# Performance work log

Hardware: AMD Instinct MI355X
Metric: run time of the kernel (lower is better)

## Reference

```python
import jax, jax.numpy as jnp
import numpy as np

NUM_HEADS = 8


def _attn(q, k, v, scale):
    # q: [B,H,Nq,d], k/v: [B,H,Nk,d]
    a = jax.nn.softmax(jnp.einsum('bhqd,bhkd->bhqk', q, k) * scale, axis=-1)
    return jnp.einsum('bhqk,bhkd->bhqd', a, v)


def setup_inputs() -> dict:
    key = jax.random.key(0)
    k1, k2, k3 = jax.random.split(key, 3)
    B, N, C = 8, 1024, 768
    x = jax.random.normal(k1, (B, N, C), dtype=jnp.float32)
    w_qkv = jax.random.normal(k2, (3 * C, C), dtype=jnp.float32) * 0.02
    w_proj = jax.random.normal(k3, (C, C), dtype=jnp.float32) * 0.02
    b_proj = jnp.zeros((C,), dtype=jnp.float32)
    return {"x": x, "w_qkv": w_qkv, "w_proj": w_proj, "b_proj": b_proj}


def reference(x, w_qkv, w_proj, b_proj):
    B, N, C = x.shape
    H = NUM_HEADS
    hd = C // H            # full head dim (scale uses this, per the source)
    g = hd // 3            # per-group head dim
    scale = hd ** (-0.5)

    qkv = (x @ w_qkv.T).reshape(B, N, 3, H, hd).transpose(2, 0, 3, 1, 4)  # [3,B,H,N,hd]
    q, k, v = qkv[0], qkv[1], qkv[2]

    q3, q4, q5 = q[..., :g], q[..., g:2 * g], q[..., 2 * g:]
    k3, k4, k5 = k[..., :g], k[..., g:2 * g], k[..., 2 * g:]
    v3, v4, v5 = v[..., :g], v[..., g:2 * g], v[..., 2 * g:]

    def merge(o):  # [B,H,N,g] -> [B,N,H*g]
        return o.transpose(0, 2, 1, 3).reshape(B, N, C // 3)

    x3 = merge(_attn(q4, jnp.concatenate([k3, k4], axis=2), jnp.concatenate([v3, v4], axis=2), scale))
    x4 = merge(_attn(q5, jnp.concatenate([k3, k5], axis=2), jnp.concatenate([v3, v5], axis=2), scale))
    x5 = merge(_attn(q5, jnp.concatenate([k4, k5], axis=2), jnp.concatenate([v4, v5], axis=2), scale))

    out = jnp.concatenate([x3, x4, x5], axis=2)
    return out @ w_proj.T + b_proj
```

## Files before the change

### kernel.cpp

```cpp
#include <hip/hip_runtime.h>
#include <hip/hip_bf16.h>

typedef unsigned short u16;
typedef __attribute__((ext_vector_type(8))) short short8;
typedef __attribute__((ext_vector_type(4))) float f32x4;
typedef __attribute__((ext_vector_type(4))) unsigned uint32x4;

__device__ __forceinline__ u16 f2b(float f) {
  unsigned u = __builtin_bit_cast(unsigned, f);
  unsigned r = u + 0x7fffu + ((u >> 16) & 1u);
  return (u16)(r >> 16);
}

__device__ __forceinline__ unsigned pkbf16(float lo, float hi) {
  unsigned r;
  asm("v_cvt_pk_bf16_f32 %0, %1, %2" : "=v"(r) : "v"(lo), "v"(hi));
  return r;
}

#define GLD_LDS16(gp, lp) __builtin_amdgcn_global_load_lds( \
    (const __attribute__((address_space(1))) void*)(gp),    \
    (__attribute__((address_space(3))) void*)(lp), 16, 0, 0)

__global__ __launch_bounds__(256) void cvt3(
    const float* __restrict__ x, const float* __restrict__ wq, const float* __restrict__ wp,
    u16* __restrict__ xb, u16* __restrict__ wqb, u16* __restrict__ wpb)
{
  const int NX = 8192 * 768 / 4, NQ = 2304 * 768 / 4, NP = 768 * 768 / 4;
  int i = blockIdx.x * 256 + threadIdx.x;
  if (i < NX) {
    float4 v = *(const float4*)&x[(size_t)i * 4];
    uint2 pk; pk.x = pkbf16(v.x, v.y); pk.y = pkbf16(v.z, v.w);
    *(uint2*)&xb[(size_t)i * 4] = pk;
  } else if (i < NX + NQ) {
    int j = i - NX;
    float sc = (j < 147456) ? 0.14724447f : 1.0f;
    float4 v = *(const float4*)&wq[(size_t)j * 4];
    uint2 pk; pk.x = pkbf16(v.x * sc, v.y * sc); pk.y = pkbf16(v.z * sc, v.w * sc);
    *(uint2*)&wqb[(size_t)j * 4] = pk;
  } else if (i < NX + NQ + NP) {
    int j = i - NX - NQ;
    int oo = (j * 4) / 768, ii = (j * 4) % 768;
    int a = ii >> 8, h = (ii >> 5) & 7, c = ii & 31;
    float4 v = *(const float4*)&wp[(size_t)j * 4];
    uint2 pk; pk.x = pkbf16(v.x, v.y); pk.y = pkbf16(v.z, v.w);
    *(uint2*)&wpb[oo * 768 + h * 96 + a * 32 + c] = pk;
  }
}

__global__ __launch_bounds__(256) void gemm_bt(
    const u16* __restrict__ A, const u16* __restrict__ Bt,
    u16* __restrict__ Cb, u16* __restrict__ vt_out, int M, int N, int K)
{
  __shared__ u16 Al[128 * 32];
  __shared__ u16 Bl[128 * 32];
  const int tid = threadIdx.x;
  const int lane = tid & 63, wave = tid >> 6;
  const int wr = wave >> 1, wc = wave & 1;
  const int g = lane >> 4, c16 = lane & 15;
  const int m0 = blockIdx.y * 128, n0 = blockIdx.x * 128;

  f32x4 acc[4][4] = {};

  const int c0 = tid, c1 = tid + 256;
  const int r0 = c0 >> 2, o0 = (c0 & 3) * 8;
  const int r1 = c1 >> 2, o1 = (c1 & 3) * 8;
  const u16* a0 = A + (size_t)(m0 + r0) * K + o0;
  const u16* a1 = A + (size_t)(m0 + r1) * K + o1;
  const u16* b0 = Bt + (size_t)(n0 + r0) * K + o0;
  const u16* b1 = Bt + (size_t)(n0 + r1) * K + o1;

  for (int k0 = 0; k0 < K; k0 += 32) {
    GLD_LDS16(a0 + k0, Al + c0 * 8);
    GLD_LDS16(a1 + k0, Al + c1 * 8);
    GLD_LDS16(b0 + k0, Bl + c0 * 8);
    GLD_LDS16(b1 + k0, Bl + c1 * 8);
    __syncthreads();
    short8 af[4], bfr[4];
#pragma unroll
    for (int m = 0; m < 4; ++m)
      af[m] = *(const short8*)&Al[(wr * 64 + m * 16 + c16) * 32 + g * 8];
#pragma unroll
    for (int n = 0; n < 4; ++n)
      bfr[n] = *(const short8*)&Bl[(wc * 64 + n * 16 + c16) * 32 + g * 8];
#pragma unroll
    for (int m = 0; m < 4; ++m)
#pragma unroll
      for (int n = 0; n < 4; ++n)
        acc[m][n] = __builtin_amdgcn_mfma_f32_16x16x32_bf16(af[m], bfr[n], acc[m][n], 0, 0, 0);
    __syncthreads();
  }

  if (vt_out && n0 >= 1536) {
#pragma unroll
    for (int m = 0; m < 4; ++m) {
      const int row0 = m0 + wr * 64 + m * 16 + g * 4;
      const int bb = row0 >> 10, nb = row0 & 1023;
      const int chunk = nb & ~31, o = nb & 31;
      const int slot0 = ((o >> 2) & 3) * 8 + ((o >> 4) & 1) * 4;
#pragma unroll
      for (int n = 0; n < 4; ++n) {
        const int colg = n0 - 1536 + wc * 64 + n * 16 + c16;
        const int hh = colg / 96, dd = colg % 96;
        uint2 pk;
        pk.x = pkbf16(acc[m][n][0], acc[m][n][1]);
        pk.y = pkbf16(acc[m][n][2], acc[m][n][3]);
        *(uint2*)&vt_out[((size_t)(bb * 8 + hh) * 96 + dd) * 1024 + chunk + slot0] = pk;
      }
    }
  } else {
#pragma unroll
    for (int m = 0; m < 4; ++m) {
      const int row = m0 + wr * 64 + m * 16 + g * 4;
#pragma unroll
      for (int n = 0; n < 4; ++n) {
        const int col = n0 + wc * 64 + n * 16 + c16;
#pragma unroll
        for (int j = 0; j < 4; ++j)
          Cb[(size_t)(row + j) * N + col] = f2b(acc[m][n][j]);
      }
    }
  }
}

__global__ __launch_bounds__(256) void gemm_bt64(
    const u16* __restrict__ A, const u16* __restrict__ Bt,
    float* __restrict__ Cf, const float* __restrict__ bias, int M, int N, int K)
{
  __shared__ u16 Al[128 * 32];
  __shared__ u16 Bl[64 * 32];
  const int tid = threadIdx.x;
  const int lane = tid & 63, wave = tid >> 6;
  const int g = lane >> 4, c16 = lane & 15;
  const int m0 = blockIdx.y * 128, n0 = blockIdx.x * 64;

  f32x4 acc[2][4] = {};

  const int c0 = tid, c1 = tid + 256;
  const int rA0 = c0 >> 2, oA0 = (c0 & 3) * 8;
  const int rA1 = c1 >> 2, oA1 = (c1 & 3) * 8;
  const u16* a0 = A + (size_t)(m0 + rA0) * K + oA0;
  const u16* a1 = A + (size_t)(m0 + rA1) * K + oA1;
  const u16* b0 = Bt + (size_t)(n0 + rA0) * K + oA0;

  for (int k0 = 0; k0 < K; k0 += 32) {
    GLD_LDS16(a0 + k0, Al + c0 * 8);
    GLD_LDS16(a1 + k0, Al + c1 * 8);
    if (tid < 256) GLD_LDS16(b0 + k0, Bl + c0 * 8);
    __syncthreads();
    short8 af[2], bfr[4];
#pragma unroll
    for (int m = 0; m < 2; ++m)
      af[m] = *(const short8*)&Al[(wave * 32 + m * 16 + c16) * 32 + g * 8];
#pragma unroll
    for (int n = 0; n < 4; ++n)
      bfr[n] = *(const short8*)&Bl[(n * 16 + c16) * 32 + g * 8];
#pragma unroll
    for (int m = 0; m < 2; ++m)
#pragma unroll
      for (int n = 0; n < 4; ++n)
        acc[m][n] = __builtin_amdgcn_mfma_f32_16x16x32_bf16(af[m], bfr[n], acc[m][n], 0, 0, 0);
    __syncthreads();
  }

#pragma unroll
  for (int m = 0; m < 2; ++m) {
    const int row = m0 + wave * 32 + m * 16 + g * 4;
#pragma unroll
    for (int n = 0; n < 4; ++n) {
      const int col = n0 + n * 16 + c16;
      const float bb = bias[col];
#pragma unroll
      for (int j = 0; j < 4; ++j)
        Cf[(size_t)(row + j) * N + col] = acc[m][n][j] + bb;
    }
  }
}

__global__ __attribute__((amdgpu_flat_work_group_size(256, 256)))
__attribute__((amdgpu_waves_per_eu(2, 4)))
void attn_kernel(
    const u16* __restrict__ qkv, const u16* __restrict__ vt, u16* __restrict__ feat)
{
  __shared__ u16 smem[2 * 2560 + 64 * 72];
  u16* Kl = smem;
  u16* Vl = smem + 2 * 2560;

  const int tid = threadIdx.x;
  const int lane = tid & 63, wave = tid >> 6;
  const int g = lane >> 4, c16 = lane & 15;
  const int id = blockIdx.x;
  const int h = id & 7;
  const int r3 = id >> 3;
  const int aidx = r3 % 3;
  const int t2 = r3 / 3;
  const int qt = t2 & 7, b = t2 >> 3;
  const int bh = b * 8 + h;
  const int q0 = qt * 128 + wave * 32;
  const size_t tb = (size_t)b * 1024;

  const int p0 = (aidx == 2) ? 1 : 0;
  const int p1 = (aidx == 0) ? 1 : 2;
  const int qoff = (aidx == 0) ? 32 : 64;

  short8 qf[2];
#pragma unroll
  for (int m = 0; m < 2; ++m)
    qf[m] = *(const short8*)&qkv[(tb + q0 + m * 16 + c16) * 2304 + h * 96 + qoff + 8 * g];

  short8 ones;
#pragma unroll
  for (int i = 0; i < 8; ++i) ones[i] = (short)0x3F80;

  f32x4 acc[2][2] = {};
  f32x4 lsv[2] = {};

  const int kkey = tid >> 2, kcc = tid & 3;
  const int vd = tid >> 3, vc = tid & 7;
  const int P[2] = { p0, p1 };
  uint4 kst[2], vst[2];
#pragma unroll
  for (int i = 0; i < 2; ++i) {
    kst[i] = *(const uint4*)&qkv[(tb + kkey) * 2304 + 768 + h * 96 + P[i] * 32 + kcc * 8];
    vst[i] = *(const uint4*)&vt[((size_t)bh * 96 + P[i] * 32 + vd) * 1024 + vc * 8];
  }

  for (int t = 0; t < 16; ++t) {
    __syncthreads();
#pragma unroll
    for (int i = 0; i < 2; ++i) {
      *(uint4*)&Kl[i * 2560 + kkey * 40 + kcc * 8] = kst[i];
      *(uint4*)&Vl[(i * 32 + vd) * 72 + vc * 8] = vst[i];
    }
    __syncthreads();
    if (t < 15) {
      int kv0 = (t + 1) * 64;
#pragma unroll
      for (int i = 0; i < 2; ++i) {
        kst[i] = *(const uint4*)&qkv[(tb + kv0 + kkey) * 2304 + 768 + h * 96 + P[i] * 32 + kcc * 8];
        vst[i] = *(const uint4*)&vt[((size_t)bh * 96 + P[i] * 32 + vd) * 1024 + kv0 + vc * 8];
      }
    }

#pragma unroll
    for (int u = 0; u < 2; ++u) {
      short8 kf[4], vf[2][2];
#pragma unroll
      for (int n = 0; n < 4; ++n)
        kf[n] = *(const short8*)&Kl[u * 2560 + (n * 16 + c16) * 40 + g * 8];
#pragma unroll
      for (int n = 0; n < 2; ++n)
#pragma unroll
        for (int kk = 0; kk < 2; ++kk)
          vf[n][kk] = *(const short8*)&Vl[(u * 32 + n * 16 + c16) * 72 + kk * 32 + g * 8];

      const f32x4 z = {0.f, 0.f, 0.f, 0.f};
#pragma unroll
      for (int m = 0; m < 2; ++m) {
        f32x4 St[4];
        __builtin_amdgcn_s_setprio(1);
#pragma unroll
        for (int n = 0; n < 4; ++n)
          St[n] = __builtin_amdgcn_mfma_f32_16x16x32_bf16(kf[n], qf[m], z, 0, 0, 0);
        __builtin_amdgcn_s_setprio(0);
        short8 pa[2];
#pragma unroll
        for (int kk = 0; kk < 2; ++kk) {
          uint32x4 w;
          w.x = pkbf16(__builtin_amdgcn_exp2f(St[2 * kk][0]),     __builtin_amdgcn_exp2f(St[2 * kk][1]));
          w.y = pkbf16(__builtin_amdgcn_exp2f(St[2 * kk][2]),     __builtin_amdgcn_exp2f(St[2 * kk][3]));
          w.z = pkbf16(__builtin_amdgcn_exp2f(St[2 * kk + 1][0]), __builtin_amdgcn_exp2f(St[2 * kk + 1][1]));
          w.w = pkbf16(__builtin_amdgcn_exp2f(St[2 * kk + 1][2]), __builtin_amdgcn_exp2f(St[2 * kk + 1][3]));
          pa[kk] = __builtin_bit_cast(short8, w);
        }
        __builtin_amdgcn_s_setprio(1);
#pragma unroll
        for (int n = 0; n < 2; ++n)
#pragma unroll
          for (int kk = 0; kk < 2; ++kk)
            acc[m][n] = __builtin_amdgcn_mfma_f32_16x16x32_bf16(pa[kk], vf[n][kk], acc[m][n], 0, 0, 0);
#pragma unroll
        for (int kk = 0; kk < 2; ++kk)
          lsv[m] = __builtin_amdgcn_mfma_f32_16x16x32_bf16(pa[kk], ones, lsv[m], 0, 0, 0);
        __builtin_amdgcn_s_setprio(0);
      }
    }
  }

  __syncthreads();
  u16* Ol = smem + wave * 1024;
#pragma unroll
  for (int m = 0; m < 2; ++m) {
    f32x4 inv;
#pragma unroll
    for (int r = 0; r < 4; ++r) inv[r] = 1.0f / lsv[m][r];
#pragma unroll
    for (int n = 0; n < 2; ++n)
#pragma unroll
      for (int r = 0; r < 4; ++r)
        Ol[(m * 16 + g * 4 + r) * 32 + n * 16 + c16] = f2b(acc[m][n][r] * inv[r]);
  }
#pragma unroll
  for (int i = 0; i < 2; ++i) {
    int idx = lane + 64 * i;
    int row = idx >> 2, q4 = idx & 3;
    uint4 val = *(const uint4*)&Ol[row * 32 + q4 * 8];
    *(uint4*)&feat[(tb + q0 + row) * 768 + h * 96 + aidx * 32 + q4 * 8] = val;
  }
}

extern "C" void kernel_launch(void* const* d_in, const int* in_sizes, int n_in,
                              void* d_out, int out_size, void* d_ws, size_t ws_size,
                              hipStream_t stream) {
  const float* x  = (const float*)d_in[0];
  const float* wq = (const float*)d_in[1];
  const float* wp = (const float*)d_in[2];
  const float* bp = (const float*)d_in[3];
  float* out = (float*)d_out;

  char* ws = (char*)d_ws;
  u16* xb    = (u16*)(ws);
  u16* wqb   = (u16*)(ws + 12582912);
  u16* wpb   = (u16*)(ws + 16121856);
  u16* qkvb  = (u16*)(ws + 17301504);
  u16* vtb   = (u16*)(ws + 55050240);
  u16* featb = xb;

  cvt3<<<8448, 256, 0, stream>>>(x, wq, wp, xb, wqb, wpb);
  gemm_bt<<<dim3(18, 64), 256, 0, stream>>>(xb, wqb, qkvb, vtb, 8192, 2304, 768);
  attn_kernel<<<1536, 256, 0, stream>>>(qkvb, vtb, featb);
  gemm_bt64<<<dim3(12, 64), 256, 0, stream>>>(featb, wpb, out, bp, 8192, 768, 768);
}
```

Measured before the change: 170.2 us.

## Load K/V fragments directly from global into registers, drop LDS staging

The attention kernel no longer stages K and V tiles through shared memory with two barriers per step. Each wave now loads its MFMA fragments straight from global memory into registers, double-buffered across the two key partitions so the next load overlaps the current compute. The waves-per-EU hint is lowered to allow more registers. In exchange, each of the four waves fetches the same K/V data separately, which raises global/L2 traffic and register pressure.

Measured after the change: 256.9 us. +50.9%, slower.

```diff
diff --git a/kernel.cpp b/kernel.cpp
--- a/kernel.cpp
+++ b/kernel.cpp
@@ -178,13 +178,11 @@
 }
 
 __global__ __attribute__((amdgpu_flat_work_group_size(256, 256)))
-__attribute__((amdgpu_waves_per_eu(2, 4)))
+__attribute__((amdgpu_waves_per_eu(2, 3)))
 void attn_kernel(
     const u16* __restrict__ qkv, const u16* __restrict__ vt, u16* __restrict__ feat)
 {
-  __shared__ u16 smem[2 * 2560 + 64 * 72];
-  u16* Kl = smem;
-  u16* Vl = smem + 2 * 2560;
+  __shared__ u16 Ols[4 * 1024];
 
   const int tid = threadIdx.x;
   const int lane = tid & 63, wave = tid >> 6;
@@ -215,80 +213,63 @@
   f32x4 acc[2][2] = {};
   f32x4 lsv[2] = {};
 
-  const int kkey = tid >> 2, kcc = tid & 3;
-  const int vd = tid >> 3, vc = tid & 7;
-  const int P[2] = { p0, p1 };
-  uint4 kst[2], vst[2];
-#pragma unroll
-  for (int i = 0; i < 2; ++i) {
-    kst[i] = *(const uint4*)&qkv[(tb + kkey) * 2304 + 768 + h * 96 + P[i] * 32 + kcc * 8];
-    vst[i] = *(const uint4*)&vt[((size_t)bh * 96 + P[i] * 32 + vd) * 1024 + vc * 8];
-  }
-
+  const size_t kRow = (tb + c16) * 2304 + 768 + h * 96 + g * 8;
+  const size_t vRowBase = ((size_t)bh * 96 + c16) * 1024 + g * 8;
+
+#define LOADSTEP(PART, KV0, KB, VB) do {                                              \
+  _Pragma("unroll")                                                                   \
+  for (int n_ = 0; n_ < 4; ++n_)                                                      \
+    KB[n_] = *(const short8*)&qkv[kRow + (size_t)((KV0) + n_ * 16) * 2304 + (PART) * 32]; \
+  _Pragma("unroll")                                                                   \
+  for (int n_ = 0; n_ < 2; ++n_)                                                      \
+    _Pragma("unroll")                                                                 \
+    for (int kk_ = 0; kk_ < 2; ++kk_)                                                 \
+      VB[n_ * 2 + kk_] = *(const short8*)&vt[vRowBase + (size_t)((PART) * 32 + n_ * 16) * 1024 + (KV0) + kk_ * 32]; \
+} while (0)
+
+#define COMPUTESTEP(KB, VB) do {                                                      \
+  const f32x4 z_ = {0.f, 0.f, 0.f, 0.f};                                              \
+  _Pragma("unroll")                                                                   \
+  for (int m_ = 0; m_ < 2; ++m_) {                                                    \
+    f32x4 St_[4];                                                                     \
+    __builtin_amdgcn_s_setprio(1);                                                    \
+    _Pragma("unroll")                                                                 \
+    for (int n_ = 0; n_ < 4; ++n_)                                                    \
+      St_[n_] = __builtin_amdgcn_mfma_f32_16x16x32_bf16(KB[n_], qf[m_], z_, 0, 0, 0); \
+    __builtin_amdgcn_s_setprio(0);                                                    \
+    short8 pa_[2];                                                                    \
+    _Pragma("unroll")                                                                 \
+    for (int kk_ = 0; kk_ < 2; ++kk_) {                                               \
+      uint32x4 w_;                                                                    \
+      w_.x = pkbf16(__builtin_amdgcn_exp2f(St_[2 * kk_][0]),     __builtin_amdgcn_exp2f(St_[2 * kk_][1]));     \
+      w_.y = pkbf16(__builtin_amdgcn_exp2f(St_[2 * kk_][2]),     __builtin_amdgcn_exp2f(St_[2 * kk_][3]));     \
+      w_.z = pkbf16(__builtin_amdgcn_exp2f(St_[2 * kk_ + 1][0]), __builtin_amdgcn_exp2f(St_[2 * kk_ + 1][1])); \
+      w_.w = pkbf16(__builtin_amdgcn_exp2f(St_[2 * kk_ + 1][2]), __builtin_amdgcn_exp2f(St_[2 * kk_ + 1][3])); \
+      pa_[kk_] = __builtin_bit_cast(short8, w_);                                      \
+    }                                                                                 \
+    __builtin_amdgcn_s_setprio(1);                                                    \
+    _Pragma("unroll")                                                                 \
+    for (int n_ = 0; n_ < 2; ++n_)                                                    \
+      _Pragma("unroll")                                                               \
+      for (int kk_ = 0; kk_ < 2; ++kk_)                                               \
+        acc[m_][n_] = __builtin_amdgcn_mfma_f32_16x16x32_bf16(pa_[kk_], VB[n_ * 2 + kk_], acc[m_][n_], 0, 0, 0); \
+    _Pragma("unroll")                                                                 \
+    for (int kk_ = 0; kk_ < 2; ++kk_)                                                 \
+      lsv[m_] = __builtin_amdgcn_mfma_f32_16x16x32_bf16(pa_[kk_], ones, lsv[m_], 0, 0, 0); \
+    __builtin_amdgcn_s_setprio(0);                                                    \
+  }                                                                                   \
+} while (0)
+
+  short8 kbA[4], vbA[4], kbB[4], vbB[4];
+  LOADSTEP(p0, 0, kbA, vbA);
   for (int t = 0; t < 16; ++t) {
-    __syncthreads();
-#pragma unroll
-    for (int i = 0; i < 2; ++i) {
-      *(uint4*)&Kl[i * 2560 + kkey * 40 + kcc * 8] = kst[i];
-      *(uint4*)&Vl[(i * 32 + vd) * 72 + vc * 8] = vst[i];
-    }
-    __syncthreads();
-    if (t < 15) {
-      int kv0 = (t + 1) * 64;
-#pragma unroll
-      for (int i = 0; i < 2; ++i) {
-        kst[i] = *(const uint4*)&qkv[(tb + kv0 + kkey) * 2304 + 768 + h * 96 + P[i] * 32 + kcc * 8];
-        vst[i] = *(const uint4*)&vt[((size_t)bh * 96 + P[i] * 32 + vd) * 1024 + kv0 + vc * 8];
-      }
-    }
-
-#pragma unroll
-    for (int u = 0; u < 2; ++u) {
-      short8 kf[4], vf[2][2];
-#pragma unroll
-      for (int n = 0; n < 4; ++n)
-        kf[n] = *(const short8*)&Kl[u * 2560 + (n * 16 + c16) * 40 + g * 8];
-#pragma unroll
-      for (int n = 0; n < 2; ++n)
-#pragma unroll
-        for (int kk = 0; kk < 2; ++kk)
-          vf[n][kk] = *(const short8*)&Vl[(u * 32 + n * 16 + c16) * 72 + kk * 32 + g * 8];
-
-      const f32x4 z = {0.f, 0.f, 0.f, 0.f};
-#pragma unroll
-      for (int m = 0; m < 2; ++m) {
-        f32x4 St[4];
-        __builtin_amdgcn_s_setprio(1);
-#pragma unroll
-        for (int n = 0; n < 4; ++n)
-          St[n] = __builtin_amdgcn_mfma_f32_16x16x32_bf16(kf[n], qf[m], z, 0, 0, 0);
-        __builtin_amdgcn_s_setprio(0);
-        short8 pa[2];
-#pragma unroll
-        for (int kk = 0; kk < 2; ++kk) {
-          uint32x4 w;
-          w.x = pkbf16(__builtin_amdgcn_exp2f(St[2 * kk][0]),     __builtin_amdgcn_exp2f(St[2 * kk][1]));
-          w.y = pkbf16(__builtin_amdgcn_exp2f(St[2 * kk][2]),     __builtin_amdgcn_exp2f(St[2 * kk][3]));
-          w.z = pkbf16(__builtin_amdgcn_exp2f(St[2 * kk + 1][0]), __builtin_amdgcn_exp2f(St[2 * kk + 1][1]));
-          w.w = pkbf16(__builtin_amdgcn_exp2f(St[2 * kk + 1][2]), __builtin_amdgcn_exp2f(St[2 * kk + 1][3]));
-          pa[kk] = __builtin_bit_cast(short8, w);
-        }
-        __builtin_amdgcn_s_setprio(1);
-#pragma unroll
-        for (int n = 0; n < 2; ++n)
-#pragma unroll
-          for (int kk = 0; kk < 2; ++kk)
-            acc[m][n] = __builtin_amdgcn_mfma_f32_16x16x32_bf16(pa[kk], vf[n][kk], acc[m][n], 0, 0, 0);
-#pragma unroll
-        for (int kk = 0; kk < 2; ++kk)
-          lsv[m] = __builtin_amdgcn_mfma_f32_16x16x32_bf16(pa[kk], ones, lsv[m], 0, 0, 0);
-        __builtin_amdgcn_s_setprio(0);
-      }
-    }
-  }
-
-  __syncthreads();
-  u16* Ol = smem + wave * 1024;
+    LOADSTEP(p1, t * 64, kbB, vbB);
+    COMPUTESTEP(kbA, vbA);
+    if (t < 15) LOADSTEP(p0, (t + 1) * 64, kbA, vbA);
+    COMPUTESTEP(kbB, vbB);
+  }
+
+  u16* Ol = Ols + wave * 1024;
 #pragma unroll
   for (int m = 0; m < 2; ++m) {
     f32x4 inv;
@@ -307,6 +288,8 @@
     uint4 val = *(const uint4*)&Ol[row * 32 + q4 * 8];
     *(uint4*)&feat[(tb + q0 + row) * 768 + h * 96 + aidx * 32 + q4 * 8] = val;
   }
+#undef LOADSTEP
+#undef COMPUTESTEP
 }
 
 extern "C" void kernel_launch(void* const* d_in, const int* in_sizes, int n_in,
```
